# Performance work log

Hardware: AMD Instinct MI355X
Metric: run time of the kernel (lower is better)

## Reference

```python
import jax, jax.numpy as jnp
import numpy as np

D_MODEL = 1024
NUM_HEADS = 16
HEAD_DIM = D_MODEL // NUM_HEADS
B, T = 4, 2048


def setup_inputs() -> dict:
    key = jax.random.key(0)
    ks = jax.random.split(key, 11)
    s = 0.02
    return {
        "q": jax.random.normal(ks[0], (B, T, D_MODEL), jnp.float32),
        "k": jax.random.normal(ks[1], (B, T, D_MODEL), jnp.float32),
        "v": jax.random.normal(ks[2], (B, T, D_MODEL), jnp.float32),
        "Wq": jax.random.normal(ks[3], (D_MODEL, D_MODEL), jnp.float32) * s,
        "bq": jnp.zeros((D_MODEL,), jnp.float32),
        "Wk": jax.random.normal(ks[4], (D_MODEL, D_MODEL), jnp.float32) * s,
        "bk": jnp.zeros((D_MODEL,), jnp.float32),
        "Wv": jax.random.normal(ks[5], (D_MODEL, D_MODEL), jnp.float32) * s,
        "bv": jnp.zeros((D_MODEL,), jnp.float32),
        "Wo": jax.random.normal(ks[6], (D_MODEL, D_MODEL), jnp.float32) * s,
        "bo": jnp.zeros((D_MODEL,), jnp.float32),
    }


def reference(q, k, v, Wq, bq, Wk, bk, Wv, bv, Wo, bo):
    Bq, Tq, _ = q.shape
    Tk = k.shape[1]
    # Linear projections then split heads: [B, H, T, Dh]
    qh = (q @ Wq + bq).reshape(Bq, Tq, NUM_HEADS, HEAD_DIM).transpose(0, 2, 1, 3)
    kh = (k @ Wk + bk).reshape(Bq, Tk, NUM_HEADS, HEAD_DIM).transpose(0, 2, 1, 3)
    vh = (v @ Wv + bv).reshape(Bq, Tk, NUM_HEADS, HEAD_DIM).transpose(0, 2, 1, 3)
    scale = 1.0 / jnp.sqrt(jnp.asarray(HEAD_DIM, qh.dtype))
    scores = jnp.einsum("bhqd,bhkd->bhqk", qh, kh) * scale  # [B,H,Tq,Tk]
    attn = jax.nn.softmax(scores, axis=-1)
    # dropout p=0.0 (eval) -> identity
    out = jnp.einsum("bhqk,bhkd->bhqd", attn, vh)  # [B,H,Tq,Dh]
    out = out.transpose(0, 2, 1, 3).reshape(Bq, Tq, D_MODEL)
    return out @ Wo + bo
```

## Files before the change

### kernel.cpp

```cpp
#include <hip/hip_runtime.h>
#include <cstdint>

#define DEV static __device__ __forceinline__

typedef unsigned short u16;
typedef unsigned int u32;
typedef __attribute__((ext_vector_type(8))) _Float16 half8;
typedef __attribute__((ext_vector_type(4))) float f32x4;
typedef __attribute__((ext_vector_type(4))) unsigned short u16x4;

DEV u16 f2h_bits(float f) {
  _Float16 h = (_Float16)f;
  union { _Float16 h; u16 u; } cv; cv.h = h; return cv.u;
}

DEV u32 pack2h(float a, float b) {
  union { __fp16 __attribute__((ext_vector_type(2))) h; u32 u; } cv;
  cv.h = __builtin_amdgcn_cvt_pkrtz(a, b);
  return cv.u;
}

#define EXP2 __builtin_amdgcn_exp2f

DEV void async_cp16(const void* g, void* l) {
  __builtin_amdgcn_global_load_lds(
      (const __attribute__((address_space(1))) void*)g,
      (__attribute__((address_space(3))) void*)l, 16, 0, 0);
}

__global__ void cvt_f16(const float4* __restrict__ in, u16* __restrict__ out) {
  const int i = blockIdx.x * 256 + threadIdx.x;
  float4 f = in[i];
  u16x4 u;
  u.x = f2h_bits(f.x); u.y = f2h_bits(f.y); u.z = f2h_bits(f.z); u.w = f2h_bits(f.w);
  *(u16x4*)(out + i * 4) = u;
}

struct TParams { const float* W[4]; u16* out[4]; };

__global__ void tcvt4(TParams p) {
  __shared__ float tile[32][33];
  const int w = blockIdx.x >> 10;
  const int bidx = blockIdx.x & 1023;
  const float* __restrict__ Wf = p.W[w];
  u16* __restrict__ Wt = p.out[w];
  const int bx = bidx & 31, by = bidx >> 5;
  const int tx = threadIdx.x & 31, ty = threadIdx.x >> 5;
#pragma unroll
  for (int r = 0; r < 32; r += 8)
    tile[ty + r][tx] = Wf[(by * 32 + ty + r) * 1024 + bx * 32 + tx];
  __syncthreads();
#pragma unroll
  for (int r = 0; r < 32; r += 8)
    Wt[(bx * 32 + ty + r) * 1024 + by * 32 + tx] = f2h_bits(tile[tx][ty + r]);
}

template<int EPI, typename OutT>
DEV void gemm_body(const u16* __restrict__ A, const u16* __restrict__ Bt,
                   const float* __restrict__ bias, OutT* __restrict__ out,
                   u16 (*As)[8192], u16 (*Bs)[8192])
{
  const int tid = threadIdx.x;
  const int wave = tid >> 6, lane = tid & 63;
  const int l15 = lane & 15, lg = lane >> 4;
  const int bid = ((blockIdx.x & 7) << 6) | (blockIdx.x >> 3);
  const int bm = bid >> 3, bn = bid & 7;
  const int m0 = bm * 128, n0 = bn * 128;
  const int wr = wave >> 1, wc = wave & 1;

  const f32x4 fz = {0.f, 0.f, 0.f, 0.f};
  f32x4 acc[4][4];
#pragma unroll
  for (int m = 0; m < 4; ++m)
#pragma unroll
    for (int n = 0; n < 4; ++n) acc[m][n] = fz;

  const char* srcA[4]; const char* srcB[4]; int dstAB[4];
#pragma unroll
  for (int j = 0; j < 4; ++j) {
    const int x = (j * 256 + tid) * 16;
    const int row = x >> 7, colb = x & 127;
    const int pc = colb ^ ((row & 7) << 4);
    srcA[j] = (const char*)A  + (size_t)(m0 + row) * 2048 + pc;
    srcB[j] = (const char*)Bt + (size_t)(n0 + row) * 2048 + pc;
    dstAB[j] = x;
  }

#define STAGE_G(buf, T)                                                     \
  do {                                                                      \
    _Pragma("unroll") for (int j = 0; j < 4; ++j)                           \
      async_cp16(srcA[j] + (size_t)(T) * 128, (char*)As[buf] + dstAB[j]);   \
    _Pragma("unroll") for (int j = 0; j < 4; ++j)                           \
      async_cp16(srcB[j] + (size_t)(T) * 128, (char*)Bs[buf] + dstAB[j]);   \
  } while (0)

  STAGE_G(0, 0);
  asm volatile("s_waitcnt vmcnt(0)" ::: "memory");
  __builtin_amdgcn_s_barrier();
  __builtin_amdgcn_sched_barrier(0);

#define GEMM_IT(T, BR, BS)                                                  \
  do {                                                                      \
    if ((T) < 15) STAGE_G(BS, (T) + 1);                                     \
    half8 af[2][4], bf[2][4];                                               \
    _Pragma("unroll") for (int kk = 0; kk < 2; ++kk)                        \
      _Pragma("unroll") for (int m = 0; m < 4; ++m) {                       \
        const int row = wr * 64 + m * 16 + l15;                             \
        af[kk][m] = *(const half8*)((const char*)As[BR] +                   \
            ((row * 128 + kk * 64 + lg * 16) ^ ((row & 7) << 4)));          \
      }                                                                     \
    _Pragma("unroll") for (int kk = 0; kk < 2; ++kk)                        \
      _Pragma("unroll") for (int n = 0; n < 4; ++n) {                       \
        const int row = wc * 64 + n * 16 + l15;                             \
        bf[kk][n] = *(const half8*)((const char*)Bs[BR] +                   \
            ((row * 128 + kk * 64 + lg * 16) ^ ((row & 7) << 4)));          \
      }                                                                     \
    _Pragma("unroll") for (int kk = 0; kk < 2; ++kk)                        \
      _Pragma("unroll") for (int m = 0; m < 4; ++m)                         \
        _Pragma("unroll") for (int n = 0; n < 4; ++n)                       \
          acc[m][n] = __builtin_amdgcn_mfma_f32_16x16x32_f16(af[kk][m], bf[kk][n], acc[m][n], 0, 0, 0); \
    if ((T) < 15) {                                                         \
      asm volatile("s_waitcnt vmcnt(0)" ::: "memory");                      \
      __builtin_amdgcn_s_barrier();                                         \
      __builtin_amdgcn_sched_barrier(0);                                    \
    }                                                                       \
  } while (0)

  for (int tb = 0; tb < 16; tb += 2) {
    GEMM_IT(tb,     0, 1);
    GEMM_IT(tb + 1, 1, 0);
  }
#undef GEMM_IT
#undef STAGE_G

#pragma unroll
  for (int m = 0; m < 4; ++m) {
    const int Rb = m0 + wr * 64 + m * 16 + lg * 4;
#pragma unroll
    for (int n = 0; n < 4; ++n) {
      const int C = n0 + wc * 64 + n * 16 + l15;
      const float bv = bias[C];
#pragma unroll
      for (int i = 0; i < 4; ++i) {
        const int R = Rb + i;
        const float vv = acc[m][n][i] + bv;
        if (EPI == 3) {
          ((float*)out)[(size_t)R * 1024 + C] = vv;
        } else {
          const int b = R >> 11, t = R & 2047, hh = C >> 6, d = C & 63;
          if (EPI == 0)
            ((u16*)out)[((b * 16 + hh) * 2048 + t) * 64 + d] = f2h_bits(vv * 0.18033688f);
          else if (EPI == 1)
            ((u16*)out)[((b * 16 + hh) * 2048 + t) * 64 + d] = f2h_bits(vv);
          else
            ((u16*)out)[((b * 16 + hh) * 64 + d) * 2048 + t] = f2h_bits(vv);
        }
      }
    }
  }
}

template<int EPI>
__launch_bounds__(256, 2)
__global__ void gemm_proj(const u16* __restrict__ A, const u16* __restrict__ Bt,
                          const float* __restrict__ bias, u16* __restrict__ out)
{
  __shared__ u16 As[2][8192];
  __shared__ u16 Bs[2][8192];
  gemm_body<EPI, u16>(A, Bt, bias, out, As, Bs);
}

__launch_bounds__(256, 2)
__global__ void gemm_o(const u16* __restrict__ A, const u16* __restrict__ Bt,
                       const float* __restrict__ bias, float* __restrict__ out)
{
  __shared__ u16 As[2][8192];
  __shared__ u16 Bs[2][8192];
  gemm_body<3, float>(A, Bt, bias, out, As, Bs);
}

__launch_bounds__(512)
__global__ void attn_kernel(const u16* __restrict__ qh, const u16* __restrict__ kh,
                            const u16* __restrict__ vt, u16* __restrict__ O)
{
  __shared__ u16 SM[32768];
  const int tid = threadIdx.x, wave = tid >> 6, lane = tid & 63;
  const int l15 = lane & 15, lg = lane >> 4;
  const int swz = ((blockIdx.x & 7) << 5) | (blockIdx.x >> 3);
  const int bh = swz >> 2;
  const int q0 = (swz & 3) << 9;
  const int b = bh >> 4, h = bh & 15;

  const char* qbase = (const char*)(qh + (size_t)(bh * 2048 + q0) * 64);
  const char* kbase = (const char*)(kh + (size_t)bh * 2048 * 64);
  const char* vbase = (const char*)(vt + (size_t)bh * 64 * 2048);

  char* Kbuf[4] = { (char*)SM,         (char*)SM + 8192,
                    (char*)SM + 16384, (char*)SM + 24576 };
  char* Vbuf[4] = { (char*)SM + 32768, (char*)SM + 40960,
                    (char*)SM + 49152, (char*)SM + 57344 };

  const bool isK = wave < 4;
  const char* ksrc[2]; int kdst[2];
  const char* vsrc[2]; int vdstA[2], vdstB[2];
#pragma unroll
  for (int j = 0; j < 2; ++j) {
    if (isK) {
      const int yb = wave * 2048 + j * 1024 + lane * 16;
      const int row = yb >> 7;
      ksrc[j] = kbase + (yb ^ ((row & 7) << 4));
      kdst[j] = yb;
      vsrc[j] = nullptr; vdstA[j] = vdstB[j] = 0;
    } else {
      const int u = (wave - 4) * 128 + j * 64 + lane;
      const int d = u >> 3, a = u & 7;
      vsrc[j] = vbase + (size_t)d * 4096 + a * 16;
      const int n = a >> 1;
      const int s1 = 32 * (n >> 1) + 16 * (a & 1) + 4 * (n & 1);
      const int sw = (d & 7) << 4;
      vdstA[j] = (d * 128 + 2 * s1) ^ sw;
      vdstB[j] = (d * 128 + 2 * s1 + 16) ^ sw;
      ksrc[j] = nullptr; kdst[j] = 0;
    }
  }

#pragma unroll
  for (int j = 0; j < 8; ++j) {
    const int x = j * 8192 + tid * 16;
    const int row = x >> 7;
    async_cp16(qbase + (x ^ ((row & 7) << 4)), (char*)SM + x);
  }
  __syncthreads();
  half8 aq[4][2];
#pragma unroll
  for (int G = 0; G < 4; ++G) {
    const int qr = wave * 64 + G * 16 + l15;
#pragma unroll
    for (int hh = 0; hh < 2; ++hh) {
      const int addr = (qr * 128 + hh * 64 + lg * 16) ^ ((qr & 7) << 4);
      aq[G][hh] = *(const half8*)((const char*)SM + addr);
    }
  }
  asm volatile("s_waitcnt lgkmcnt(0)" ::: "memory");
  __syncthreads();

  uint4 va[2][2];
  if (isK) {
    async_cp16(ksrc[0], Kbuf[0] + kdst[0]);
    async_cp16(ksrc[1], Kbuf[0] + kdst[1]);
    async_cp16(ksrc[0] + 8192, Kbuf[1] + kdst[0]);
    async_cp16(ksrc[1] + 8192, Kbuf[1] + kdst[1]);
    asm volatile("s_waitcnt vmcnt(0)" ::: "memory");
  } else {
#pragma unroll
    for (int tt = 0; tt < 2; ++tt)
#pragma unroll
      for (int j = 0; j < 2; ++j) {
        uint4 v = *(const uint4*)(vsrc[j] + (size_t)tt * 128);
        uint2 w0; w0.x = v.x; w0.y = v.y;
        uint2 w1; w1.x = v.z; w1.y = v.w;
        *(uint2*)(Vbuf[tt] + vdstA[j]) = w0;
        *(uint2*)(Vbuf[tt] + vdstB[j]) = w1;
      }
#pragma unroll
    for (int j = 0; j < 2; ++j) {
      va[0][j] = *(const uint4*)(vsrc[j] + 2 * 128);
      va[1][j] = *(const uint4*)(vsrc[j] + 3 * 128);
    }
    asm volatile("s_waitcnt lgkmcnt(0)" ::: "memory");
  }
  __builtin_amdgcn_s_barrier();
  __builtin_amdgcn_sched_barrier(0);

  half8 ones;
#pragma unroll
  for (int i = 0; i < 8; ++i) ones[i] = (_Float16)1.0f;

  const f32x4 fz = {0.f, 0.f, 0.f, 0.f};
  f32x4 o[4][4], osum[4];
#pragma unroll
  for (int i = 0; i < 4; ++i) {
#pragma unroll
    for (int G = 0; G < 4; ++G) o[i][G] = fz;
    osum[i] = fz;
  }

#define ATTN_TILE(BT)                                                           \
  do {                                                                          \
    half8 pa[4][2];                                                             \
    _Pragma("unroll") for (int hp = 0; hp < 2; ++hp) {                          \
      f32x4 s0[4], s1[4];                                                       \
      __builtin_amdgcn_s_setprio(1);                                            \
      {                                                                         \
        const int krow = (2 * hp) * 16 + l15;                                   \
        const int a0 = (krow * 128 + lg * 16) ^ ((krow & 7) << 4);              \
        half8 bk0 = *(const half8*)(Kbuf[BT] + a0);                             \
        half8 bk1 = *(const half8*)(Kbuf[BT] + (a0 ^ 64));                      \
        _Pragma("unroll") for (int G = 0; G < 4; ++G) {                         \
          s0[G] = __builtin_amdgcn_mfma_f32_16x16x32_f16(bk0, aq[G][0], fz, 0, 0, 0); \
          s0[G] = __builtin_amdgcn_mfma_f32_16x16x32_f16(bk1, aq[G][1], s0[G], 0, 0, 0); \
        }                                                                       \
      }                                                                         \
      {                                                                         \
        const int krow = (2 * hp + 1) * 16 + l15;                               \
        const int a0 = (krow * 128 + lg * 16) ^ ((krow & 7) << 4);              \
        half8 bk0 = *(const half8*)(Kbuf[BT] + a0);                             \
        half8 bk1 = *(const half8*)(Kbuf[BT] + (a0 ^ 64));                      \
        _Pragma("unroll") for (int G = 0; G < 4; ++G) {                         \
          s1[G] = __builtin_amdgcn_mfma_f32_16x16x32_f16(bk0, aq[G][0], fz, 0, 0, 0); \
          s1[G] = __builtin_amdgcn_mfma_f32_16x16x32_f16(bk1, aq[G][1], s1[G], 0, 0, 0); \
        }                                                                       \
      }                                                                         \
      __builtin_amdgcn_s_setprio(0);                                            \
      _Pragma("unroll") for (int G = 0; G < 4; ++G) {                           \
        union { u32 w[4]; half8 hv; } cv;                                       \
        cv.w[0] = pack2h(EXP2(s0[G][0]), EXP2(s0[G][1]));                       \
        cv.w[1] = pack2h(EXP2(s0[G][2]), EXP2(s0[G][3]));                       \
        cv.w[2] = pack2h(EXP2(s1[G][0]), EXP2(s1[G][1]));                       \
        cv.w[3] = pack2h(EXP2(s1[G][2]), EXP2(s1[G][3]));                       \
        pa[G][hp] = cv.hv;                                                      \
      }                                                                         \
    }                                                                           \
    __builtin_amdgcn_s_setprio(1);                                              \
    _Pragma("unroll") for (int G = 0; G < 4; ++G) {                             \
      osum[G] = __builtin_amdgcn_mfma_f32_16x16x32_f16(pa[G][0], ones, osum[G], 0, 0, 0); \
      osum[G] = __builtin_amdgcn_mfma_f32_16x16x32_f16(pa[G][1], ones, osum[G], 0, 0, 0); \
    }                                                                           \
    _Pragma("unroll") for (int nd = 0; nd < 4; ++nd) {                          \
      const int dr = nd * 16 + l15;                                             \
      const int a0 = (dr * 128 + lg * 16) ^ ((dr & 7) << 4);                    \
      half8 bv0 = *(const half8*)(Vbuf[BT] + a0);                               \
      half8 bv1 = *(const half8*)(Vbuf[BT] + (a0 ^ 64));                        \
      _Pragma("unroll") for (int G = 0; G < 4; ++G) {                           \
        o[nd][G] = __builtin_amdgcn_mfma_f32_16x16x32_f16(pa[G][0], bv0, o[nd][G], 0, 0, 0); \
        o[nd][G] = __builtin_amdgcn_mfma_f32_16x16x32_f16(pa[G][1], bv1, o[nd][G], 0, 0, 0); \
      }                                                                         \
    }                                                                           \
    __builtin_amdgcn_s_setprio(0);                                              \
  } while (0)

#define PERIOD(P, C0, C1, S0, S1, DOSTAGE, DOVA, DOBAR)                         \
  do {                                                                          \
    if (isK) {                                                                  \
      if (DOSTAGE) {                                                            \
        async_cp16(ksrc[0] + (size_t)(2*(P)+2) * 8192, Kbuf[S0] + kdst[0]);     \
        async_cp16(ksrc[1] + (size_t)(2*(P)+2) * 8192, Kbuf[S0] + kdst[1]);     \
        async_cp16(ksrc[0] + (size_t)(2*(P)+3) * 8192, Kbuf[S1] + kdst[0]);     \
        async_cp16(ksrc[1] + (size_t)(2*(P)+3) * 8192, Kbuf[S1] + kdst[1]);     \
      }                                                                         \
    } else {                                                                    \
      if (DOSTAGE) {                                                            \
        _Pragma("unroll") for (int j = 0; j < 2; ++j) {                         \
          uint2 w0, w1;                                                         \
          w0.x = va[0][j].x; w0.y = va[0][j].y;                                 \
          w1.x = va[0][j].z; w1.y = va[0][j].w;                                 \
          *(uint2*)(Vbuf[S0] + vdstA[j]) = w0;                                  \
          *(uint2*)(Vbuf[S0] + vdstB[j]) = w1;                                  \
          w0.x = va[1][j].x; w0.y = va[1][j].y;                                 \
          w1.x = va[1][j].z; w1.y = va[1][j].w;                                 \
          *(uint2*)(Vbuf[S1] + vdstA[j]) = w0;                                  \
          *(uint2*)(Vbuf[S1] + vdstB[j]) = w1;                                  \
        }                                                                       \
        if (DOVA) {                                                             \
          _Pragma("unroll") for (int j = 0; j < 2; ++j) {                       \
            va[0][j] = *(const uint4*)(vsrc[j] + (size_t)(2*(P)+4) * 128);      \
            va[1][j] = *(const uint4*)(vsrc[j] + (size_t)(2*(P)+5) * 128);      \
          }                                                                     \
        }                                                                       \
      }                                                                         \
    }                                                                           \
    ATTN_TILE(C0);                                                              \
    ATTN_TILE(C1);                                                              \
    if (DOBAR) {                                                                \
      if (isK) asm volatile("s_waitcnt vmcnt(0)" ::: "memory");                 \
      else     asm volatile("s_waitcnt lgkmcnt(0)" ::: "memory");               \
      __builtin_amdgcn_s_barrier();                                             \
      __builtin_amdgcn_sched_barrier(0);                                        \
    }                                                                           \
  } while (0)

  for (int pb = 0; pb < 14; pb += 2) {
    PERIOD(pb,     0, 1, 2, 3, 1, 1, 1);
    PERIOD(pb + 1, 2, 3, 0, 1, 1, 1, 1);
  }
  PERIOD(14, 0, 1, 2, 3, 1, 0, 1);
  PERIOD(15, 2, 3, 0, 1, 0, 0, 0);
#undef PERIOD
#undef ATTN_TILE

#pragma unroll
  for (int G = 0; G < 4; ++G)
#pragma unroll
    for (int i = 0; i < 4; ++i) {
      const float inv = 1.f / osum[G][i];
      const int t = q0 + wave * 64 + G * 16 + lg * 4 + i;
      u16* orow = O + ((size_t)(b * 2048 + t)) * 1024 + h * 64;
#pragma unroll
      for (int nd = 0; nd < 4; ++nd)
        orow[nd * 16 + l15] = f2h_bits(o[nd][G][i] * inv);
    }
}

extern "C" void kernel_launch(void* const* d_in, const int* in_sizes, int n_in,
                              void* d_out, int out_size, void* d_ws, size_t ws_size,
                              hipStream_t stream)
{
  const float* q  = (const float*)d_in[0];
  const float* k  = (const float*)d_in[1];
  const float* v  = (const float*)d_in[2];
  const float* Wq = (const float*)d_in[3];
  const float* bq = (const float*)d_in[4];
  const float* Wk = (const float*)d_in[5];
  const float* bk = (const float*)d_in[6];
  const float* Wv = (const float*)d_in[7];
  const float* bv = (const float*)d_in[8];
  const float* Wo = (const float*)d_in[9];
  const float* bo = (const float*)d_in[10];

  u16* W = (u16*)d_ws;
  const unsigned MB = 1u << 20;
  u16* wtq = W + 0 * MB;
  u16* wtk = W + 1 * MB;
  u16* wtv = W + 2 * MB;
  u16* wto = W + 3 * MB;
  u16* qhb = W + 4 * MB;
  u16* khb = W + 12 * MB;
  u16* vtb = W + 20 * MB;
  u16* Xb  = W + 28 * MB;

  TParams tp;
  tp.W[0] = Wq; tp.W[1] = Wk; tp.W[2] = Wv; tp.W[3] = Wo;
  tp.out[0] = wtq; tp.out[1] = wtk; tp.out[2] = wtv; tp.out[3] = wto;
  tcvt4<<<4096, 256, 0, stream>>>(tp);

  cvt_f16<<<8192, 256, 0, stream>>>((const float4*)q, Xb);
  gemm_proj<0><<<512, 256, 0, stream>>>(Xb, wtq, bq, qhb);
  cvt_f16<<<8192, 256, 0, stream>>>((const float4*)k, Xb);
  gemm_proj<1><<<512, 256, 0, stream>>>(Xb, wtk, bk, khb);
  cvt_f16<<<8192, 256, 0, stream>>>((const float4*)v, Xb);
  gemm_proj<2><<<512, 256, 0, stream>>>(Xb, wtv, bv, vtb);

  attn_kernel<<<256, 512, 0, stream>>>(qhb, khb, vtb, Xb);

  gemm_o<<<512, 256, 0, stream>>>(Xb, wto, bo, (float*)d_out);
}
```

Baseline: 200.2 us.

## Use 256x128 GEMM tiles with 512 threads and triple-buffered async loads

After: 200.7 us. Within noise of the previous version (+0.2%).

```diff
diff --git a/kernel.cpp b/kernel.cpp
--- a/kernel.cpp
+++ b/kernel.cpp
@@ -58,14 +58,14 @@
 template<int EPI, typename OutT>
 DEV void gemm_body(const u16* __restrict__ A, const u16* __restrict__ Bt,
                    const float* __restrict__ bias, OutT* __restrict__ out,
-                   u16 (*As)[8192], u16 (*Bs)[8192])
+                   u16 (*As)[16384], u16 (*Bs)[8192])
 {
   const int tid = threadIdx.x;
   const int wave = tid >> 6, lane = tid & 63;
   const int l15 = lane & 15, lg = lane >> 4;
-  const int bid = ((blockIdx.x & 7) << 6) | (blockIdx.x >> 3);
+  const int bid = ((blockIdx.x & 7) << 5) | (blockIdx.x >> 3);
   const int bm = bid >> 3, bn = bid & 7;
-  const int m0 = bm * 128, n0 = bn * 128;
+  const int m0 = bm * 256, n0 = bn * 128;
   const int wr = wave >> 1, wc = wave & 1;
 
   const f32x4 fz = {0.f, 0.f, 0.f, 0.f};
@@ -75,33 +75,42 @@
 #pragma unroll
     for (int n = 0; n < 4; ++n) acc[m][n] = fz;
 
-  const char* srcA[4]; const char* srcB[4]; int dstAB[4];
+  const char* srcA[4]; int dstA[4];
+  const char* srcB[2]; int dstB[2];
 #pragma unroll
   for (int j = 0; j < 4; ++j) {
-    const int x = (j * 256 + tid) * 16;
+    const int x = (j * 512 + tid) * 16;
     const int row = x >> 7, colb = x & 127;
     const int pc = colb ^ ((row & 7) << 4);
-    srcA[j] = (const char*)A  + (size_t)(m0 + row) * 2048 + pc;
+    srcA[j] = (const char*)A + (size_t)(m0 + row) * 2048 + pc;
+    dstA[j] = x;
+  }
+#pragma unroll
+  for (int j = 0; j < 2; ++j) {
+    const int x = (j * 512 + tid) * 16;
+    const int row = x >> 7, colb = x & 127;
+    const int pc = colb ^ ((row & 7) << 4);
     srcB[j] = (const char*)Bt + (size_t)(n0 + row) * 2048 + pc;
-    dstAB[j] = x;
+    dstB[j] = x;
   }
 
 #define STAGE_G(buf, T)                                                     \
   do {                                                                      \
     _Pragma("unroll") for (int j = 0; j < 4; ++j)                           \
-      async_cp16(srcA[j] + (size_t)(T) * 128, (char*)As[buf] + dstAB[j]);   \
-    _Pragma("unroll") for (int j = 0; j < 4; ++j)                           \
-      async_cp16(srcB[j] + (size_t)(T) * 128, (char*)Bs[buf] + dstAB[j]);   \
+      async_cp16(srcA[j] + (size_t)(T) * 128, (char*)As[buf] + dstA[j]);    \
+    _Pragma("unroll") for (int j = 0; j < 2; ++j)                           \
+      async_cp16(srcB[j] + (size_t)(T) * 128, (char*)Bs[buf] + dstB[j]);    \
   } while (0)
 
   STAGE_G(0, 0);
-  asm volatile("s_waitcnt vmcnt(0)" ::: "memory");
+  STAGE_G(1, 1);
+  asm volatile("s_waitcnt vmcnt(6)" ::: "memory");
   __builtin_amdgcn_s_barrier();
   __builtin_amdgcn_sched_barrier(0);
 
-#define GEMM_IT(T, BR, BS)                                                  \
+#define GEMM_IT(T, BR, BS, DOSTAGE, DOBAR, CNT)                             \
   do {                                                                      \
-    if ((T) < 15) STAGE_G(BS, (T) + 1);                                     \
+    if (DOSTAGE) STAGE_G(BS, (T) + 2);                                      \
     half8 af[2][4], bf[2][4];                                               \
     _Pragma("unroll") for (int kk = 0; kk < 2; ++kk)                        \
       _Pragma("unroll") for (int m = 0; m < 4; ++m) {                       \
@@ -119,17 +128,23 @@
       _Pragma("unroll") for (int m = 0; m < 4; ++m)                         \
         _Pragma("unroll") for (int n = 0; n < 4; ++n)                       \
           acc[m][n] = __builtin_amdgcn_mfma_f32_16x16x32_f16(af[kk][m], bf[kk][n], acc[m][n], 0, 0, 0); \
-    if ((T) < 15) {                                                         \
-      asm volatile("s_waitcnt vmcnt(0)" ::: "memory");                      \
+    if (DOBAR) {                                                            \
+      if (CNT) asm volatile("s_waitcnt vmcnt(6)" ::: "memory");             \
+      else     asm volatile("s_waitcnt vmcnt(0)" ::: "memory");             \
       __builtin_amdgcn_s_barrier();                                         \
       __builtin_amdgcn_sched_barrier(0);                                    \
     }                                                                       \
   } while (0)
 
-  for (int tb = 0; tb < 16; tb += 2) {
-    GEMM_IT(tb,     0, 1);
-    GEMM_IT(tb + 1, 1, 0);
-  }
+  for (int tb = 0; tb < 12; tb += 3) {
+    GEMM_IT(tb,     0, 2, 1, 1, 1);
+    GEMM_IT(tb + 1, 1, 0, 1, 1, 1);
+    GEMM_IT(tb + 2, 2, 1, 1, 1, 1);
+  }
+  GEMM_IT(12, 0, 2, 1, 1, 1);
+  GEMM_IT(13, 1, 0, 1, 1, 1);
+  GEMM_IT(14, 2, 1, 0, 1, 0);
+  GEMM_IT(15, 0, 1, 0, 0, 0);
 #undef GEMM_IT
 #undef STAGE_G
 
@@ -161,21 +176,21 @@
 }
 
 template<int EPI>
-__launch_bounds__(256, 2)
+__launch_bounds__(512)
 __global__ void gemm_proj(const u16* __restrict__ A, const u16* __restrict__ Bt,
                           const float* __restrict__ bias, u16* __restrict__ out)
 {
-  __shared__ u16 As[2][8192];
-  __shared__ u16 Bs[2][8192];
+  __shared__ u16 As[3][16384];
+  __shared__ u16 Bs[3][8192];
   gemm_body<EPI, u16>(A, Bt, bias, out, As, Bs);
 }
 
-__launch_bounds__(256, 2)
+__launch_bounds__(512)
 __global__ void gemm_o(const u16* __restrict__ A, const u16* __restrict__ Bt,
                        const float* __restrict__ bias, float* __restrict__ out)
 {
-  __shared__ u16 As[2][8192];
-  __shared__ u16 Bs[2][8192];
+  __shared__ u16 As[3][16384];
+  __shared__ u16 Bs[3][8192];
   gemm_body<3, float>(A, Bt, bias, out, As, Bs);
 }
 
@@ -434,13 +449,13 @@
   tcvt4<<<4096, 256, 0, stream>>>(tp);
 
   cvt_f16<<<8192, 256, 0, stream>>>((const float4*)q, Xb);
-  gemm_proj<0><<<512, 256, 0, stream>>>(Xb, wtq, bq, qhb);
+  gemm_proj<0><<<256, 512, 0, stream>>>(Xb, wtq, bq, qhb);
   cvt_f16<<<8192, 256, 0, stream>>>((const float4*)k, Xb);
-  gemm_proj<1><<<512, 256, 0, stream>>>(Xb, wtk, bk, khb);
+  gemm_proj<1><<<256, 512, 0, stream>>>(Xb, wtk, bk, khb);
   cvt_f16<<<8192, 256, 0, stream>>>((const float4*)v, Xb);
-  gemm_proj<2><<<512, 256, 0, stream>>>(Xb, wtv, bv, vtb);
+  gemm_proj<2><<<256, 512, 0, stream>>>(Xb, wtv, bv, vtb);
 
   attn_kernel<<<256, 512, 0, stream>>>(qhb, khb, vtb, Xb);
 
-  gemm_o<<<512, 256, 0, stream>>>(Xb, wto, bo, (float*)d_out);
-}
+  gemm_o<<<256, 512, 0, stream>>>(Xb, wto, bo, (float*)d_out);
+}
```
